# Optimization experiments

Measured on AMD Instinct MI355X. Metric: run time of the kernel, lower is better.

Reference implementation:

```python
import jax, jax.numpy as jnp
import numpy as np

B, S, D, H, SPAN = 4, 1024, 768, 12, 512
HD = D // H  # 64


def setup_inputs() -> dict:
    key = jax.random.key(0)
    ks = jax.random.split(key, 8)
    hidden_states = jax.random.normal(ks[0], (B, S, D), jnp.float32)
    rel_embeddings = jax.random.normal(ks[1], (2 * SPAN, D), jnp.float32) * 0.02
    Wq = jax.random.normal(ks[2], (D, D), jnp.float32) * 0.02
    Wk = jax.random.normal(ks[3], (D, D), jnp.float32) * 0.02
    Wv = jax.random.normal(ks[4], (D, D), jnp.float32) * 0.02
    Wo = jax.random.normal(ks[5], (D, D), jnp.float32) * 0.02
    bq = jnp.zeros((D,), jnp.float32); bk = jnp.zeros((D,), jnp.float32)
    bv = jnp.zeros((D,), jnp.float32); bo = jnp.zeros((D,), jnp.float32)
    ln_g = jnp.ones((D,), jnp.float32); ln_b = jnp.zeros((D,), jnp.float32)
    idx = jnp.arange(S)
    relative_pos = (idx[:, None] - idx[None, :]).astype(jnp.int32)  # q - k
    lengths = jnp.array([1024, 896, 768, 512])  # padding-style mask
    valid = idx[None, :] < lengths[:, None]  # [B,S]
    attention_mask = (valid[:, :, None] & valid[:, None, :])[:, None, :, :].astype(jnp.int32)  # [B,1,S,S]
    return dict(hidden_states=hidden_states, rel_embeddings=rel_embeddings,
                Wq=Wq, bq=bq, Wk=Wk, bk=bk, Wv=Wv, bv=bv, Wo=Wo, bo=bo,
                ln_g=ln_g, ln_b=ln_b, attention_mask=attention_mask,
                relative_pos=relative_pos)


def reference(hidden_states, rel_embeddings, Wq, bq, Wk, bk, Wv, bv, Wo, bo,
              ln_g, ln_b, attention_mask, relative_pos):
    # content projections -> [B,H,S,HD]
    q = (hidden_states @ Wq.T + bq).reshape(B, S, H, HD).transpose(0, 2, 1, 3)
    k = (hidden_states @ Wk.T + bk).reshape(B, S, H, HD).transpose(0, 2, 1, 3)
    v = (hidden_states @ Wv.T + bv).reshape(B, S, H, HD).transpose(0, 2, 1, 3)

    scale_qk = jnp.sqrt(jnp.float32(HD * 3))  # scale_factor = 3
    scores = jnp.einsum('bhqd,bhkd->bhqk', q, k) / scale_qk

    # shared-key position projections -> [H, 2*SPAN, HD]
    pos_q = (rel_embeddings @ Wq.T + bq).reshape(2 * SPAN, H, HD).transpose(1, 0, 2)
    pos_k = (rel_embeddings @ Wk.T + bk).reshape(2 * SPAN, H, HD).transpose(1, 0, 2)

    rp = relative_pos.astype(jnp.int32)
    # c2p: query vs relative key-position embedding, gathered by clamp(rel+span)
    c2p_att = jnp.einsum('bhqd,hkd->bhqk', q, pos_k)  # [B,H,S,2*SPAN]
    c2p_pos = jnp.clip(rp + SPAN, 0, 2 * SPAN - 1)
    c2p_idx = jnp.broadcast_to(c2p_pos[None, None], (B, H, S, S))
    c2p = jnp.take_along_axis(c2p_att, c2p_idx, axis=-1) / scale_qk

    # p2c: key vs relative query-position embedding, gathered by clamp(-rel+span), then transposed
    p2c_att = jnp.einsum('bhkd,hqd->bhkq', k, pos_q)  # [B,H,S,2*SPAN]
    p2c_pos = jnp.clip(SPAN - rp, 0, 2 * SPAN - 1)
    p2c_idx = jnp.broadcast_to(p2c_pos[None, None], (B, H, S, S))
    p2c = jnp.swapaxes(jnp.take_along_axis(p2c_att, p2c_idx, axis=-1), -1, -2)
    p2c = p2c / jnp.sqrt(jnp.float32(HD))  # note: torch uses sqrt(d) here, no scale_factor

    scores = scores + c2p + p2c

    # XSoftmax: masked softmax with zeros at masked positions
    mask = attention_mask.astype(bool)  # [B,1,S,S]
    neg = jnp.finfo(scores.dtype).min
    probs = jax.nn.softmax(jnp.where(mask, scores, neg), axis=-1)
    probs = jnp.where(mask, probs, jnp.float32(0))

    ctx = jnp.einsum('bhqk,bhkd->bhqd', probs, v).transpose(0, 2, 1, 3).reshape(B, S, D)

    # DebertaV2SelfOutput: dense + residual + LayerNorm(eps=1e-7)
    x = ctx @ Wo.T + bo + hidden_states
    mu = x.mean(-1, keepdims=True)
    var = ((x - mu) ** 2).mean(-1, keepdims=True)
    return (x - mu) / jnp.sqrt(var + 1e-7) * ln_g + ln_b
```

## Files before the change

### kernel.cpp

```cpp
#include <hip/hip_runtime.h>
#include <hip/hip_bf16.h>
#include <stdint.h>

typedef __hip_bfloat16 bf16;
typedef __attribute__((ext_vector_type(8))) short s8v;
typedef __attribute__((ext_vector_type(4))) float f4v;

__device__ __align__(16) bf16 g_hidden[4096 * 768];
__device__ __align__(16) bf16 g_rel[1024 * 768];
__device__ __align__(16) bf16 g_Wqkv[2304 * 768];
__device__ __align__(16) bf16 g_Wo[768 * 768];
__device__ __align__(16) bf16 g_biasQKV[2304];
__device__ __align__(16) bf16 g_biasPos[1536];
__device__ __align__(16) bf16 g_bo[768];
__device__ __align__(16) bf16 g_lng[768];
__device__ __align__(16) bf16 g_lnb[768];
__device__ __align__(16) bf16 g_Y1[4096 * 1536];
__device__ __align__(16) bf16 g_VT[48u * 64 * 1024];
__device__ __align__(16) bf16 g_Yp[1024 * 1536];
__device__ __align__(16) bf16 g_ctx[4096 * 768];
__device__ __align__(16) float g_X[4096 * 768];
__device__ int g_vq[4096], g_vk[4096], g_kmax[4];

__device__ __forceinline__ float bfs(short x) {
  return __uint_as_float(((unsigned int)(unsigned short)x) << 16);
}
__device__ __forceinline__ unsigned short f2bf(float f) {
  bf16 h = __float2bfloat16(f);
  return *(unsigned short*)&h;
}
__device__ __forceinline__ bool detect_bf16(const void* lng_raw) {
  return *(const unsigned int*)lng_raw == 0x3F803F80u;
}

__device__ __forceinline__ void cvt4(const void* src, bf16* dst, long grp, bool isbf) {
  long e = grp * 4;
  if (isbf) {
    *(uint2*)(dst + e) = *(const uint2*)((const bf16*)src + e);
  } else {
    float4 f = *(const float4*)((const float*)src + e);
    union { unsigned short us[4]; uint2 v; } u;
    u.us[0] = f2bf(f.x); u.us[1] = f2bf(f.y); u.us[2] = f2bf(f.z); u.us[3] = f2bf(f.w);
    *(uint2*)(dst + e) = u.v;
  }
}

__global__ __launch_bounds__(256) void cvt_inputs(
    const void* h, const void* r,
    const void* wq, const void* wk, const void* wv, const void* wo,
    const void* bq, const void* bk, const void* bv, const void* bo,
    const void* lg, const void* lb)
{
  if (blockIdx.x == 0 && threadIdx.x < 4) g_kmax[threadIdx.x] = 0;
  const bool isbf = detect_bf16(lg);
  long i = (long)blockIdx.x * 256 + threadIdx.x;
  if (i < 786432) { cvt4(h,  g_hidden,          i, isbf); return; } i -= 786432;
  if (i < 196608) { cvt4(r,  g_rel,             i, isbf); return; } i -= 196608;
  if (i < 147456) { cvt4(wq, g_Wqkv,            i, isbf); return; } i -= 147456;
  if (i < 147456) { cvt4(wk, g_Wqkv + 589824,   i, isbf); return; } i -= 147456;
  if (i < 147456) { cvt4(wv, g_Wqkv + 1179648,  i, isbf); return; } i -= 147456;
  if (i < 147456) { cvt4(wo, g_Wo,              i, isbf); return; } i -= 147456;
  if (i < 192)    { cvt4(bq, g_biasQKV,         i, isbf); return; } i -= 192;
  if (i < 192)    { cvt4(bk, g_biasQKV + 768,   i, isbf); return; } i -= 192;
  if (i < 192)    { cvt4(bv, g_biasQKV + 1536,  i, isbf); return; } i -= 192;
  if (i < 192)    { cvt4(bq, g_biasPos,         i, isbf); return; } i -= 192;
  if (i < 192)    { cvt4(bk, g_biasPos + 768,   i, isbf); return; } i -= 192;
  if (i < 192)    { cvt4(lg, g_lng,             i, isbf); return; } i -= 192;
  if (i < 192)    { cvt4(lb, g_lnb,             i, isbf); return; }
}

__global__ __launch_bounds__(256) void mask_prep(const int* __restrict__ mask) {
  int t = blockIdx.x * 256 + threadIdx.x;
  int b = t >> 10, i = t & 1023;
  int vq = mask[((size_t)(b * 1024 + i)) * 1024];
  int vk = mask[((size_t)(b * 1024)) * 1024 + i];
  g_vq[t] = vq;
  g_vk[t] = vk;
  if (vq | vk) atomicMax(&g_kmax[b], i + 1);
}

__global__ __launch_bounds__(256, 2) void gemm_bt(int which) {
  __shared__ short As[128][72];
  __shared__ short Bs[128][72];

  const bf16 *A, *B; const bf16* bias;
  int lda, ldb, K, mode;
  const int m0 = blockIdx.y * 128, n0 = blockIdx.x * 128;

  if (which == 0) {
    A = g_hidden; lda = 768; B = g_Wqkv; ldb = 768; bias = g_biasQKV; K = 768;
    mode = (n0 >= 1536) ? 5 : 0;
  } else if (which == 1) {
    A = g_rel; lda = 768; B = g_Wqkv; ldb = 768; bias = g_biasPos; K = 768; mode = 1;
  } else {
    A = g_ctx; lda = 768; B = g_Wo; ldb = 768; bias = g_bo; K = 768; mode = 4;
  }

  const int tid = threadIdx.x, wave = tid >> 6, lane = tid & 63;
  const int quad = lane >> 4, l15 = lane & 15;
  const int wm = (wave >> 1) * 64, wn = (wave & 1) * 64;
  const int sr = tid >> 2, sc8 = (tid & 3) * 16;

  f4v acc[4][4];
#pragma unroll
  for (int i = 0; i < 4; i++)
#pragma unroll
    for (int j = 0; j < 4; j++) acc[i][j] = (f4v){0.f, 0.f, 0.f, 0.f};

  uint4 pa0, pa1, pa2, pa3, pb0, pb1, pb2, pb3;
#define LOAD_T(k0)                                                           \
  {                                                                          \
    const bf16* ap = A + (size_t)(m0 + sr) * lda + (k0) + sc8;               \
    const bf16* ap2 = A + (size_t)(m0 + sr + 64) * lda + (k0) + sc8;         \
    const bf16* bp = B + (size_t)(n0 + sr) * ldb + (k0) + sc8;               \
    const bf16* bp2 = B + (size_t)(n0 + sr + 64) * ldb + (k0) + sc8;         \
    pa0 = *(const uint4*)ap;  pa1 = *(const uint4*)(ap + 8);                 \
    pa2 = *(const uint4*)ap2; pa3 = *(const uint4*)(ap2 + 8);                \
    pb0 = *(const uint4*)bp;  pb1 = *(const uint4*)(bp + 8);                 \
    pb2 = *(const uint4*)bp2; pb3 = *(const uint4*)(bp2 + 8);                \
  }

  LOAD_T(0)
  for (int k0 = 0; k0 < K; k0 += 64) {
    __syncthreads();
    *(uint4*)&As[sr][sc8] = pa0;      *(uint4*)&As[sr][sc8 + 8] = pa1;
    *(uint4*)&As[sr + 64][sc8] = pa2; *(uint4*)&As[sr + 64][sc8 + 8] = pa3;
    *(uint4*)&Bs[sr][sc8] = pb0;      *(uint4*)&Bs[sr][sc8 + 8] = pb1;
    *(uint4*)&Bs[sr + 64][sc8] = pb2; *(uint4*)&Bs[sr + 64][sc8 + 8] = pb3;
    if (k0 + 64 < K) LOAD_T(k0 + 64)
    __syncthreads();

    s8v af[4][2], bfr[4][2];
#pragma unroll
    for (int mt = 0; mt < 4; mt++) {
      af[mt][0] = *(const s8v*)&As[wm + mt * 16 + l15][quad * 8];
      af[mt][1] = *(const s8v*)&As[wm + mt * 16 + l15][32 + quad * 8];
    }
#pragma unroll
    for (int nt = 0; nt < 4; nt++) {
      bfr[nt][0] = *(const s8v*)&Bs[wn + nt * 16 + l15][quad * 8];
      bfr[nt][1] = *(const s8v*)&Bs[wn + nt * 16 + l15][32 + quad * 8];
    }
#pragma unroll
    for (int mt = 0; mt < 4; mt++)
#pragma unroll
      for (int nt = 0; nt < 4; nt++) {
        acc[mt][nt] = __builtin_amdgcn_mfma_f32_16x16x32_bf16(af[mt][0], bfr[nt][0], acc[mt][nt], 0, 0, 0);
        acc[mt][nt] = __builtin_amdgcn_mfma_f32_16x16x32_bf16(af[mt][1], bfr[nt][1], acc[mt][nt], 0, 0, 0);
      }
  }
#undef LOAD_T

  float biasv[4];
#pragma unroll
  for (int nt = 0; nt < 4; nt++)
    biasv[nt] = bfs(*(const short*)&bias[n0 + wn + nt * 16 + l15]);

#pragma unroll
  for (int mt = 0; mt < 4; mt++) {
#pragma unroll
    for (int nt = 0; nt < 4; nt++) {
      const int mbase = m0 + wm + mt * 16 + quad * 4;
      const int n = n0 + wn + nt * 16 + l15;
      if (mode == 5) {
        const int dd = n - 1536, hv = dd >> 6, hd = dd & 63;
        const int bb = mbase >> 10, ss = mbase & 1023;
        float t0 = acc[mt][nt][0] + biasv[nt], t1 = acc[mt][nt][1] + biasv[nt];
        float t2 = acc[mt][nt][2] + biasv[nt], t3 = acc[mt][nt][3] + biasv[nt];
        uint2 pk;
        pk.x = (unsigned int)f2bf(t0) | ((unsigned int)f2bf(t1) << 16);
        pk.y = (unsigned int)f2bf(t2) | ((unsigned int)f2bf(t3) << 16);
        *(uint2*)(g_VT + (((size_t)(bb * 12 + hv) * 64 + hd) << 10) + ss) = pk;
        continue;
      }
#pragma unroll
      for (int reg = 0; reg < 4; reg++) {
        const int m = mbase + reg;
        float v = acc[mt][nt][reg] + biasv[nt];
        if (mode == 0) {
          g_Y1[(size_t)m * 1536 + n] = __float2bfloat16(v);
        } else if (mode == 1) {
          g_Yp[(size_t)m * 1536 + n] = __float2bfloat16(v);
        } else {
          v += bfs(*(const short*)&g_hidden[(size_t)m * 768 + n]);
          g_X[(size_t)m * 768 + n] = v;
        }
      }
    }
  }
}

__global__ __launch_bounds__(256, 2) void attn_mfma() {
  const int bh = blockIdx.y, b = bh / 12, hh = bh - b * 12;
  const int q0 = blockIdx.x * 64;
  const int tid = threadIdx.x, wave = tid >> 6, lane = tid & 63;
  const int quad = lane >> 4, l15 = lane & 15;
  const int kmax = g_kmax[b];

  if (q0 >= kmax) {
    uint4 zz = {0u, 0u, 0u, 0u};
#pragma unroll
    for (int s = tid; s < 512; s += 256) {
      int r = s >> 3, cc = (s & 7) * 8;
      *(uint4*)(g_ctx + (size_t)(b * 1024 + q0 + r) * 768 + hh * 64 + cc) = zz;
    }
    return;
  }

  __shared__ short Ks[64][72], VTs[64][72];
  __shared__ short BandA[128][72];
  __shared__ short BandB[128][72];
  __shared__ short Pl[4][16][72];
  short* C2Pl = &BandA[0][0];
  short* P2Cl = &BandB[0][0];

  const size_t qrow = (size_t)(b * 1024 + q0 + wave * 16 + l15) * 1536 + hh * 64;
  const s8v qf0 = *(const s8v*)(g_Y1 + qrow + quad * 8);
  const s8v qf1 = *(const s8v*)(g_Y1 + qrow + 32 + quad * 8);

  int vqr[4];
#pragma unroll
  for (int reg = 0; reg < 4; reg++)
    vqr[reg] = g_vq[b * 1024 + q0 + wave * 16 + quad * 4 + reg];

  f4v accO[4];
#pragma unroll
  for (int dt = 0; dt < 4; dt++) accO[dt] = (f4v){0.f, 0.f, 0.f, 0.f};
  float psum[4] = {0.f, 0.f, 0.f, 0.f};

  const int sr = tid >> 2, sc8 = (tid & 3) * 16;
  const int brow = tid >> 1, bcol = (tid & 1) * 32;
  const bf16* Kbase = g_Y1 + (size_t)(b * 1024) * 1536 + 768 + hh * 64;
  const bf16* Vbase = g_VT + ((size_t)bh << 16);
  const bf16* PKbase = g_Yp + 768 + hh * 64;
  const bf16* PQbase = g_Yp + hh * 64;

  uint4 rk0, rk1, rv0, rv1, rpk[4], rpq[4];
#define LOAD_A(k0)                                                         \
  {                                                                        \
    const bf16* kp = Kbase + (size_t)((k0) + sr) * 1536 + sc8;             \
    rk0 = *(const uint4*)kp; rk1 = *(const uint4*)(kp + 8);                \
    const bf16* vp = Vbase + ((size_t)sr << 10) + (k0) + sc8;              \
    rv0 = *(const uint4*)vp; rv1 = *(const uint4*)(vp + 8);                \
    int jk = min(max(q0 - (k0) + 449 + brow, 0), 1023);                    \
    const bf16* pk = PKbase + (size_t)jk * 1536 + bcol;                    \
    rpk[0] = *(const uint4*)pk;       rpk[1] = *(const uint4*)(pk + 8);    \
    rpk[2] = *(const uint4*)(pk + 16); rpk[3] = *(const uint4*)(pk + 24);  \
    int jq = min(max((k0) - q0 + 449 + brow, 0), 1023);                    \
    const bf16* pq = PQbase + (size_t)jq * 1536 + bcol;                    \
    rpq[0] = *(const uint4*)pq;       rpq[1] = *(const uint4*)(pq + 8);    \
    rpq[2] = *(const uint4*)(pq + 16); rpq[3] = *(const uint4*)(pq + 24);  \
  }

  LOAD_A(0)
  const float r192 = 0.0721687836487032f;
  const float r64 = 0.125f;

  for (int k0 = 0; k0 < kmax; k0 += 64) {
    __syncthreads();
    *(uint4*)&Ks[sr][sc8] = rk0;   *(uint4*)&Ks[sr][sc8 + 8] = rk1;
    *(uint4*)&VTs[sr][sc8] = rv0;  *(uint4*)&VTs[sr][sc8 + 8] = rv1;
    *(uint4*)&BandA[brow][bcol] = rpk[0];      *(uint4*)&BandA[brow][bcol + 8] = rpk[1];
    *(uint4*)&BandA[brow][bcol + 16] = rpk[2]; *(uint4*)&BandA[brow][bcol + 24] = rpk[3];
    *(uint4*)&BandB[brow][bcol] = rpq[0];      *(uint4*)&BandB[brow][bcol + 8] = rpq[1];
    *(uint4*)&BandB[brow][bcol + 16] = rpq[2]; *(uint4*)&BandB[brow][bcol + 24] = rpq[3];
    if (k0 + 64 < kmax) LOAD_A(k0 + 64)
    __syncthreads();

    const s8v ka0 = *(const s8v*)&Ks[wave * 16 + l15][quad * 8];
    const s8v ka1 = *(const s8v*)&Ks[wave * 16 + l15][32 + quad * 8];

    f4v cacc[8], pacc[8];
#pragma unroll
    for (int nt2 = 0; nt2 < 8; nt2++) {
      s8v b0 = *(const s8v*)&BandA[nt2 * 16 + l15][quad * 8];
      s8v b1 = *(const s8v*)&BandA[nt2 * 16 + l15][32 + quad * 8];
      cacc[nt2] = __builtin_amdgcn_mfma_f32_16x16x32_bf16(qf0, b0, (f4v){0.f, 0.f, 0.f, 0.f}, 0, 0, 0);
      cacc[nt2] = __builtin_amdgcn_mfma_f32_16x16x32_bf16(qf1, b1, cacc[nt2], 0, 0, 0);
      s8v c0 = *(const s8v*)&BandB[nt2 * 16 + l15][quad * 8];
      s8v c1 = *(const s8v*)&BandB[nt2 * 16 + l15][32 + quad * 8];
      pacc[nt2] = __builtin_amdgcn_mfma_f32_16x16x32_bf16(ka0, c0, (f4v){0.f, 0.f, 0.f, 0.f}, 0, 0, 0);
      pacc[nt2] = __builtin_amdgcn_mfma_f32_16x16x32_bf16(ka1, c1, pacc[nt2], 0, 0, 0);
    }

    f4v sacc[4];
#pragma unroll
    for (int nt = 0; nt < 4; nt++) {
      s8v kb0 = *(const s8v*)&Ks[nt * 16 + l15][quad * 8];
      s8v kb1 = *(const s8v*)&Ks[nt * 16 + l15][32 + quad * 8];
      sacc[nt] = __builtin_amdgcn_mfma_f32_16x16x32_bf16(qf0, kb0, (f4v){0.f, 0.f, 0.f, 0.f}, 0, 0, 0);
      sacc[nt] = __builtin_amdgcn_mfma_f32_16x16x32_bf16(qf1, kb1, sacc[nt], 0, 0, 0);
    }

    __syncthreads();
#pragma unroll
    for (int nt2 = 0; nt2 < 8; nt2++) {
      const int col = nt2 * 16 + l15;
#pragma unroll
      for (int reg = 0; reg < 4; reg++) {
        const int row = wave * 16 + quad * 4 + reg;
        C2Pl[row * 130 + col] = (short)f2bf(cacc[nt2][reg]);
        P2Cl[row * 130 + col] = (short)f2bf(pacc[nt2][reg]);
      }
    }
    __syncthreads();

    const bool tail = (k0 + 64 > kmax);
#pragma unroll
    for (int nt = 0; nt < 4; nt++) {
      const int kl = nt * 16 + l15;
#pragma unroll
      for (int reg = 0; reg < 4; reg++) {
        const int ql = wave * 16 + quad * 4 + reg;
        float c2 = bfs(C2Pl[ql * 130 + (ql - kl + 63)]);
        float p2 = bfs(P2Cl[kl * 130 + (kl - ql + 63)]);
        float sc = (sacc[nt][reg] + c2) * r192 + p2 * r64;
        float pe = __expf(fminf(sc, 60.f));
        if (tail && (k0 + kl >= kmax)) pe = 0.f;
        psum[reg] += pe;
        Pl[wave][quad * 4 + reg][kl] = (short)f2bf(pe);
      }
    }

    s8v pa0 = *(const s8v*)&Pl[wave][l15][quad * 8];
    s8v pa1 = *(const s8v*)&Pl[wave][l15][32 + quad * 8];
#pragma unroll
    for (int dt = 0; dt < 4; dt++) {
      s8v vb0 = *(const s8v*)&VTs[dt * 16 + l15][quad * 8];
      s8v vb1 = *(const s8v*)&VTs[dt * 16 + l15][32 + quad * 8];
      accO[dt] = __builtin_amdgcn_mfma_f32_16x16x32_bf16(pa0, vb0, accO[dt], 0, 0, 0);
      accO[dt] = __builtin_amdgcn_mfma_f32_16x16x32_bf16(pa1, vb1, accO[dt], 0, 0, 0);
    }
  }
#undef LOAD_A

#pragma unroll
  for (int off = 1; off < 16; off <<= 1)
#pragma unroll
    for (int reg = 0; reg < 4; reg++) psum[reg] += __shfl_xor(psum[reg], off);

  float inv[4];
#pragma unroll
  for (int reg = 0; reg < 4; reg++)
    inv[reg] = (vqr[reg] != 0 && psum[reg] > 0.f) ? 1.f / psum[reg] : 0.f;

#pragma unroll
  for (int dt = 0; dt < 4; dt++)
#pragma unroll
    for (int reg = 0; reg < 4; reg++) {
      float v = accO[dt][reg] * inv[reg];
      g_ctx[(size_t)(b * 1024 + q0 + wave * 16 + quad * 4 + reg) * 768 + hh * 64 + dt * 16 + l15] =
          __float2bfloat16(v);
    }
}

__global__ __launch_bounds__(256) void ln_kernel(const void* lng_raw, void* out) {
  const bool isbf = detect_bf16(lng_raw);
  const int row = blockIdx.x;
  const int tid = threadIdx.x;
  const float* xr = g_X + (size_t)row * 768;
  float x0 = xr[tid], x1 = xr[tid + 256], x2 = xr[tid + 512];
  float s = x0 + x1 + x2;
  float s2 = x0 * x0 + x1 * x1 + x2 * x2;
#pragma unroll
  for (int off = 32; off; off >>= 1) { s += __shfl_xor(s, off); s2 += __shfl_xor(s2, off); }
  __shared__ float red[2][4];
  int w = tid >> 6, ln = tid & 63;
  if (ln == 0) { red[0][w] = s; red[1][w] = s2; }
  __syncthreads();
  float ts = red[0][0] + red[0][1] + red[0][2] + red[0][3];
  float ts2 = red[1][0] + red[1][1] + red[1][2] + red[1][3];
  float mu = ts * (1.f / 768.f);
  float var = fmaxf(ts2 * (1.f / 768.f) - mu * mu, 0.f);
  float rstd = rsqrtf(var + 1e-7f);
#pragma unroll
  for (int q = 0; q < 3; q++) {
    int cidx = tid + q * 256;
    float xv = (q == 0) ? x0 : (q == 1 ? x1 : x2);
    float gg = bfs(*(const short*)&g_lng[cidx]);
    float bb = bfs(*(const short*)&g_lnb[cidx]);
    float val = (xv - mu) * rstd * gg + bb;
    if (isbf) ((bf16*)out)[(size_t)row * 768 + cidx] = __float2bfloat16(val);
    else      ((float*)out)[(size_t)row * 768 + cidx] = val;
  }
}

extern "C" void kernel_launch(void* const* d_in, const int* in_sizes, int n_in,
                              void* d_out, int out_size, void* d_ws, size_t ws_size,
                              hipStream_t stream) {
  const int* amask = (const int*)d_in[12];
  (void)d_ws; (void)ws_size; (void)in_sizes; (void)n_in; (void)out_size;

  cvt_inputs<<<dim3(6150), 256, 0, stream>>>(
      d_in[0], d_in[1], d_in[2], d_in[4], d_in[6], d_in[8],
      d_in[3], d_in[5], d_in[7], d_in[9], d_in[10], d_in[11]);
  mask_prep<<<dim3(16), 256, 0, stream>>>(amask);
  gemm_bt<<<dim3(18, 32, 1), 256, 0, stream>>>(0);
  gemm_bt<<<dim3(12, 8, 1), 256, 0, stream>>>(1);
  attn_mfma<<<dim3(16, 48), 256, 0, stream>>>();
  gemm_bt<<<dim3(6, 32, 1), 256, 0, stream>>>(4);
  ln_kernel<<<dim3(4096), 256, 0, stream>>>(d_in[10], d_out);
}
```

Baseline: 382.5 us.

## Compute only needed band diagonals and read K/V directly from global

Each wave now computes only the 5 band tiles (80 rows) its 16 queries actually touch instead of all 8, which cuts c2p/p2c MFMA work. K and V tiles are no longer staged through LDS; the fragments are loaded directly from global memory inside the loop. LDS drops from the K/V buffers, and launch bounds rise to 3 blocks per CU for more occupancy. In exchange the K/V reads become uncoalesced and unprefetched global loads on the critical path, and register pressure under the tighter bound may cause spills.

```diff
diff --git a/kernel.cpp b/kernel.cpp
--- a/kernel.cpp
+++ b/kernel.cpp
@@ -190,7 +190,7 @@
   }
 }
 
-__global__ __launch_bounds__(256, 2) void attn_mfma() {
+__global__ __launch_bounds__(256, 3) void attn_mfma() {
   const int bh = blockIdx.y, b = bh / 12, hh = bh - b * 12;
   const int q0 = blockIdx.x * 64;
   const int tid = threadIdx.x, wave = tid >> 6, lane = tid & 63;
@@ -207,12 +207,11 @@
     return;
   }
 
-  __shared__ short Ks[64][72], VTs[64][72];
-  __shared__ short BandA[128][72];
-  __shared__ short BandB[128][72];
+  __shared__ short BandPK[128][72];
+  __shared__ short BandPQ[128][72];
   __shared__ short Pl[4][16][72];
-  short* C2Pl = &BandA[0][0];
-  short* P2Cl = &BandB[0][0];
+  short* C2Pr = &BandPK[0][0];
+  short* P2Cr = &BandPQ[0][0];
 
   const size_t qrow = (size_t)(b * 1024 + q0 + wave * 16 + l15) * 1536 + hh * 64;
   const s8v qf0 = *(const s8v*)(g_Y1 + qrow + quad * 8);
@@ -228,79 +227,75 @@
   for (int dt = 0; dt < 4; dt++) accO[dt] = (f4v){0.f, 0.f, 0.f, 0.f};
   float psum[4] = {0.f, 0.f, 0.f, 0.f};
 
-  const int sr = tid >> 2, sc8 = (tid & 3) * 16;
-  const int brow = tid >> 1, bcol = (tid & 1) * 32;
   const bf16* Kbase = g_Y1 + (size_t)(b * 1024) * 1536 + 768 + hh * 64;
   const bf16* Vbase = g_VT + ((size_t)bh << 16);
   const bf16* PKbase = g_Yp + 768 + hh * 64;
   const bf16* PQbase = g_Yp + hh * 64;
 
-  uint4 rk0, rk1, rv0, rv1, rpk[4], rpq[4];
-#define LOAD_A(k0)                                                         \
-  {                                                                        \
-    const bf16* kp = Kbase + (size_t)((k0) + sr) * 1536 + sc8;             \
-    rk0 = *(const uint4*)kp; rk1 = *(const uint4*)(kp + 8);                \
-    const bf16* vp = Vbase + ((size_t)sr << 10) + (k0) + sc8;              \
-    rv0 = *(const uint4*)vp; rv1 = *(const uint4*)(vp + 8);                \
-    int jk = min(max(q0 - (k0) + 449 + brow, 0), 1023);                    \
-    const bf16* pk = PKbase + (size_t)jk * 1536 + bcol;                    \
-    rpk[0] = *(const uint4*)pk;       rpk[1] = *(const uint4*)(pk + 8);    \
-    rpk[2] = *(const uint4*)(pk + 16); rpk[3] = *(const uint4*)(pk + 24);  \
-    int jq = min(max((k0) - q0 + 449 + brow, 0), 1023);                    \
-    const bf16* pq = PQbase + (size_t)jq * 1536 + bcol;                    \
-    rpq[0] = *(const uint4*)pq;       rpq[1] = *(const uint4*)(pq + 8);    \
-    rpq[2] = *(const uint4*)(pq + 16); rpq[3] = *(const uint4*)(pq + 24);  \
-  }
-
-  LOAD_A(0)
+  const int brow = tid >> 1, bcol = (tid & 1) * 32;
+  uint4 rpk[4], rpq[4];
+#define LOAD_B(k0)                                                          \
+  {                                                                         \
+    int jk = min(max(q0 - (k0) + 449 + brow, 0), 1023);                     \
+    const bf16* pk = PKbase + (size_t)jk * 1536 + bcol;                     \
+    rpk[0] = *(const uint4*)pk;        rpk[1] = *(const uint4*)(pk + 8);    \
+    rpk[2] = *(const uint4*)(pk + 16); rpk[3] = *(const uint4*)(pk + 24);   \
+    int jq = min(max((k0) - q0 + 449 + brow, 0), 1023);                     \
+    const bf16* pq = PQbase + (size_t)jq * 1536 + bcol;                     \
+    rpq[0] = *(const uint4*)pq;        rpq[1] = *(const uint4*)(pq + 8);    \
+    rpq[2] = *(const uint4*)(pq + 16); rpq[3] = *(const uint4*)(pq + 24);   \
+  }
+
+  LOAD_B(0)
   const float r192 = 0.0721687836487032f;
   const float r64 = 0.125f;
 
   for (int k0 = 0; k0 < kmax; k0 += 64) {
     __syncthreads();
-    *(uint4*)&Ks[sr][sc8] = rk0;   *(uint4*)&Ks[sr][sc8 + 8] = rk1;
-    *(uint4*)&VTs[sr][sc8] = rv0;  *(uint4*)&VTs[sr][sc8 + 8] = rv1;
-    *(uint4*)&BandA[brow][bcol] = rpk[0];      *(uint4*)&BandA[brow][bcol + 8] = rpk[1];
-    *(uint4*)&BandA[brow][bcol + 16] = rpk[2]; *(uint4*)&BandA[brow][bcol + 24] = rpk[3];
-    *(uint4*)&BandB[brow][bcol] = rpq[0];      *(uint4*)&BandB[brow][bcol + 8] = rpq[1];
-    *(uint4*)&BandB[brow][bcol + 16] = rpq[2]; *(uint4*)&BandB[brow][bcol + 24] = rpq[3];
-    if (k0 + 64 < kmax) LOAD_A(k0 + 64)
-    __syncthreads();
-
-    const s8v ka0 = *(const s8v*)&Ks[wave * 16 + l15][quad * 8];
-    const s8v ka1 = *(const s8v*)&Ks[wave * 16 + l15][32 + quad * 8];
-
-    f4v cacc[8], pacc[8];
-#pragma unroll
-    for (int nt2 = 0; nt2 < 8; nt2++) {
-      s8v b0 = *(const s8v*)&BandA[nt2 * 16 + l15][quad * 8];
-      s8v b1 = *(const s8v*)&BandA[nt2 * 16 + l15][32 + quad * 8];
-      cacc[nt2] = __builtin_amdgcn_mfma_f32_16x16x32_bf16(qf0, b0, (f4v){0.f, 0.f, 0.f, 0.f}, 0, 0, 0);
-      cacc[nt2] = __builtin_amdgcn_mfma_f32_16x16x32_bf16(qf1, b1, cacc[nt2], 0, 0, 0);
-      s8v c0 = *(const s8v*)&BandB[nt2 * 16 + l15][quad * 8];
-      s8v c1 = *(const s8v*)&BandB[nt2 * 16 + l15][32 + quad * 8];
-      pacc[nt2] = __builtin_amdgcn_mfma_f32_16x16x32_bf16(ka0, c0, (f4v){0.f, 0.f, 0.f, 0.f}, 0, 0, 0);
-      pacc[nt2] = __builtin_amdgcn_mfma_f32_16x16x32_bf16(ka1, c1, pacc[nt2], 0, 0, 0);
-    }
+    *(uint4*)&BandPK[brow][bcol] = rpk[0];      *(uint4*)&BandPK[brow][bcol + 8] = rpk[1];
+    *(uint4*)&BandPK[brow][bcol + 16] = rpk[2]; *(uint4*)&BandPK[brow][bcol + 24] = rpk[3];
+    *(uint4*)&BandPQ[brow][bcol] = rpq[0];      *(uint4*)&BandPQ[brow][bcol + 8] = rpq[1];
+    *(uint4*)&BandPQ[brow][bcol + 16] = rpq[2]; *(uint4*)&BandPQ[brow][bcol + 24] = rpq[3];
+    if (k0 + 64 < kmax) LOAD_B(k0 + 64)
+    __syncthreads();
+
+    const bf16* karow = Kbase + (size_t)(k0 + wave * 16 + l15) * 1536;
+    const s8v ka0 = *(const s8v*)(karow + quad * 8);
+    const s8v ka1 = *(const s8v*)(karow + 32 + quad * 8);
 
     f4v sacc[4];
 #pragma unroll
     for (int nt = 0; nt < 4; nt++) {
-      s8v kb0 = *(const s8v*)&Ks[nt * 16 + l15][quad * 8];
-      s8v kb1 = *(const s8v*)&Ks[nt * 16 + l15][32 + quad * 8];
+      const bf16* kbrow = Kbase + (size_t)(k0 + nt * 16 + l15) * 1536;
+      s8v kb0 = *(const s8v*)(kbrow + quad * 8);
+      s8v kb1 = *(const s8v*)(kbrow + 32 + quad * 8);
       sacc[nt] = __builtin_amdgcn_mfma_f32_16x16x32_bf16(qf0, kb0, (f4v){0.f, 0.f, 0.f, 0.f}, 0, 0, 0);
       sacc[nt] = __builtin_amdgcn_mfma_f32_16x16x32_bf16(qf1, kb1, sacc[nt], 0, 0, 0);
     }
 
-    __syncthreads();
-#pragma unroll
-    for (int nt2 = 0; nt2 < 8; nt2++) {
-      const int col = nt2 * 16 + l15;
+    f4v cacc[5], pacc[5];
+#pragma unroll
+    for (int t2 = 0; t2 < 5; t2++) {
+      const int nr = (wave + t2) * 16 + l15;
+      s8v b0 = *(const s8v*)&BandPK[nr][quad * 8];
+      s8v b1 = *(const s8v*)&BandPK[nr][32 + quad * 8];
+      cacc[t2] = __builtin_amdgcn_mfma_f32_16x16x32_bf16(qf0, b0, (f4v){0.f, 0.f, 0.f, 0.f}, 0, 0, 0);
+      cacc[t2] = __builtin_amdgcn_mfma_f32_16x16x32_bf16(qf1, b1, cacc[t2], 0, 0, 0);
+      s8v c0 = *(const s8v*)&BandPQ[nr][quad * 8];
+      s8v c1 = *(const s8v*)&BandPQ[nr][32 + quad * 8];
+      pacc[t2] = __builtin_amdgcn_mfma_f32_16x16x32_bf16(ka0, c0, (f4v){0.f, 0.f, 0.f, 0.f}, 0, 0, 0);
+      pacc[t2] = __builtin_amdgcn_mfma_f32_16x16x32_bf16(ka1, c1, pacc[t2], 0, 0, 0);
+    }
+
+    __syncthreads();
+#pragma unroll
+    for (int t2 = 0; t2 < 5; t2++) {
+      const int col = t2 * 16 + l15;
 #pragma unroll
       for (int reg = 0; reg < 4; reg++) {
         const int row = wave * 16 + quad * 4 + reg;
-        C2Pl[row * 130 + col] = (short)f2bf(cacc[nt2][reg]);
-        P2Cl[row * 130 + col] = (short)f2bf(pacc[nt2][reg]);
+        C2Pr[row * 88 + col] = (short)f2bf(cacc[t2][reg]);
+        P2Cr[row * 88 + col] = (short)f2bf(pacc[t2][reg]);
       }
     }
     __syncthreads();
@@ -311,14 +306,14 @@
       const int kl = nt * 16 + l15;
 #pragma unroll
       for (int reg = 0; reg < 4; reg++) {
-        const int ql = wave * 16 + quad * 4 + reg;
-        float c2 = bfs(C2Pl[ql * 130 + (ql - kl + 63)]);
-        float p2 = bfs(P2Cl[kl * 130 + (kl - ql + 63)]);
+        const int qr = quad * 4 + reg;
+        float c2 = bfs(C2Pr[(wave * 16 + qr) * 88 + qr - kl + 63]);
+        float p2 = bfs(P2Cr[kl * 88 + l15 - wave * 16 - qr + 63]);
         float sc = (sacc[nt][reg] + c2) * r192 + p2 * r64;
         float pe = __expf(fminf(sc, 60.f));
         if (tail && (k0 + kl >= kmax)) pe = 0.f;
         psum[reg] += pe;
-        Pl[wave][quad * 4 + reg][kl] = (short)f2bf(pe);
+        Pl[wave][qr][kl] = (short)f2bf(pe);
       }
     }
 
@@ -326,13 +321,14 @@
     s8v pa1 = *(const s8v*)&Pl[wave][l15][32 + quad * 8];
 #pragma unroll
     for (int dt = 0; dt < 4; dt++) {
-      s8v vb0 = *(const s8v*)&VTs[dt * 16 + l15][quad * 8];
-      s8v vb1 = *(const s8v*)&VTs[dt * 16 + l15][32 + quad * 8];
+      const bf16* vrow = Vbase + ((size_t)(dt * 16 + l15) << 10) + k0;
+      s8v vb0 = *(const s8v*)(vrow + quad * 8);
+      s8v vb1 = *(const s8v*)(vrow + 32 + quad * 8);
       accO[dt] = __builtin_amdgcn_mfma_f32_16x16x32_bf16(pa0, vb0, accO[dt], 0, 0, 0);
       accO[dt] = __builtin_amdgcn_mfma_f32_16x16x32_bf16(pa1, vb1, accO[dt], 0, 0, 0);
     }
   }
-#undef LOAD_A
+#undef LOAD_B
 
 #pragma unroll
   for (int off = 1; off < 16; off <<= 1)
```

After: 440.5 us. +15.2%, slower.
